# Kernel optimization log

Hardware: AMD Instinct MI355X
Metric: run time of the kernel (lower is better)

## Reference

```python
import jax, jax.numpy as jnp
import numpy as np

TAU = 1.0
SCALE = 0.5
LN_EPS = 1e-5
NORM_EPS = 1e-12


def setup_inputs() -> dict:
    key = jax.random.key(0)
    k1, = jax.random.split(key, 1)
    N, D = 16384, 128
    x = jax.random.normal(k1, (N, D), dtype=jnp.float32)
    gamma = jnp.ones((D,), dtype=jnp.float32)
    beta = jnp.zeros((D,), dtype=jnp.float32)
    return {"x": x, "gamma": gamma, "beta": beta}


def reference(x, gamma, beta):
    # 'cn' branch: row-normalize, full pairwise cosine sim, row softmax, aggregate
    norm = jnp.sqrt(jnp.sum(x * x, axis=1, keepdims=True))
    norm_x = x / jnp.maximum(norm, NORM_EPS)          # [N, D]
    sim = jax.nn.softmax(norm_x @ norm_x.T / TAU, axis=1)  # [N, N]
    x_neg = sim @ x                                    # [N, D]
    y = (1.0 + SCALE) * x - SCALE * x_neg
    # LayerNorm over the hidden dim
    mu = jnp.mean(y, axis=-1, keepdims=True)
    var = jnp.mean((y - mu) ** 2, axis=-1, keepdims=True)
    return (y - mu) * jax.lax.rsqrt(var + LN_EPS) * gamma + beta
```

## Files before the change

### kernel.cpp

```cpp
#include <hip/hip_runtime.h>
#include <stdint.h>

#define NN 16384
#define DD 128
#define KT 64
#define QB 256

typedef __bf16 bf16x8 __attribute__((ext_vector_type(8)));
typedef float f32x16 __attribute__((ext_vector_type(16)));
typedef uint32_t u32x4 __attribute__((ext_vector_type(4)));

using gv = __attribute__((address_space(1))) const void;
using lv = __attribute__((address_space(3))) void;

__device__ __forceinline__ uint16_t f2bf(float f) {
  uint32_t u = __builtin_bit_cast(uint32_t, f);
  u += 0x7fffu + ((u >> 16) & 1u);
  return (uint16_t)(u >> 16);
}

__global__ void k_norm(const float* __restrict__ x, uint16_t* __restrict__ nx) {
  const int wave = threadIdx.x >> 6, lane = threadIdx.x & 63;
  const int row = blockIdx.x * 4 + wave;
  const float2 v = *reinterpret_cast<const float2*>(x + (size_t)row * DD + 2 * lane);
  float ss = v.x * v.x + v.y * v.y;
#pragma unroll
  for (int m = 1; m < 64; m <<= 1) ss += __shfl_xor(ss, m);
  const float rn = 1.0f / fmaxf(sqrtf(ss), 1e-12f);
  uint32_t w = (uint32_t)f2bf(v.x * rn) | ((uint32_t)f2bf(v.y * rn) << 16);
  *reinterpret_cast<uint32_t*>(nx + (size_t)row * DD + 2 * lane) = w;
}

__global__ void k_transpose(const float* __restrict__ x, uint16_t* __restrict__ xT) {
  __shared__ uint16_t tile[64 * 65];
  const int r0 = (blockIdx.x >> 1) * 64;
  const int c0 = (blockIdx.x & 1) * 64;
  const int t = threadIdx.x;
#pragma unroll
  for (int e = 0; e < 16; ++e) {
    int idx = e * 256 + t;
    int r = idx >> 6, c = idx & 63;
    tile[r * 65 + c] = f2bf(x[(size_t)(r0 + r) * DD + c0 + c]);
  }
  __syncthreads();
#pragma unroll
  for (int e = 0; e < 16; ++e) {
    int idx = e * 256 + t;
    int cc = idx >> 6, rr = idx & 63;
    xT[(size_t)(c0 + cc) * NN + r0 + rr] = tile[rr * 65 + cc];
  }
}

__global__ __launch_bounds__(512, 2) void k_attn(
    const uint16_t* __restrict__ nx, const uint16_t* __restrict__ xT,
    float* __restrict__ Op, float* __restrict__ Lp, int nsplit) {
  __shared__ alignas(16) uint16_t Kb[3][KT * DD];
  __shared__ alignas(16) uint16_t Vb[3][DD * KT];

  const int tid = threadIdx.x;
  const int wave = tid >> 6;
  const int lane = tid & 63;
  const int rl = lane & 31;
  const int hi = lane >> 5;
  const int cswz = (16 * hi) ^ ((lane & 7) << 4);

  const int id = blockIdx.x;
  int qblock, split;
  if (nsplit == 4) { split = (id & 7) >> 1; qblock = ((id >> 3) << 1) | (id & 1); }
  else { qblock = id & 63; split = id >> 6; }

  const int nt = (NN / KT) / nsplit;
  const int t0s = split * nt;
  const int qw = qblock * QB + wave * 32;

  bf16x8 q8[8];
#pragma unroll
  for (int dc = 0; dc < 8; ++dc)
    q8[dc] = *reinterpret_cast<const bf16x8*>(
        nx + (size_t)(qw + rl) * DD + dc * 16 + 8 * hi);

  f32x16 o[4];
#pragma unroll
  for (int dt = 0; dt < 4; ++dt)
#pragma unroll
    for (int r = 0; r < 16; ++r) o[dt][r] = 0.f;
  float lsum = 0.f;

  const char* nxb = reinterpret_cast<const char*>(nx);
  const char* xtb = reinterpret_cast<const char*>(xT);

  auto stage = [&](int tt, int buf) {
    const int k0 = tt * KT;
#pragma unroll
    for (int jj = 0; jj < 2; ++jj) {
      const int j = wave * 2 + jj;
      const int A = j * 1024 + lane * 16;
      {
        const int row = A >> 8, b = A & 255;
        const char* src = nxb + (size_t)(k0 + row) * 256 + (b ^ ((row & 7) << 4));
        __builtin_amdgcn_global_load_lds((gv*)src,
            (lv*)(reinterpret_cast<char*>(&Kb[buf][0]) + j * 1024), 16, 0, 0);
      }
      {
        const int d = A >> 7, b2 = A & 127;
        const char* src = xtb + (size_t)d * (NN * 2) + (size_t)k0 * 2 + (b2 ^ ((d & 7) << 4));
        __builtin_amdgcn_global_load_lds((gv*)src,
            (lv*)(reinterpret_cast<char*>(&Vb[buf][0]) + j * 1024), 16, 0, 0);
      }
    }
  };

  stage(t0s + 0, 0);
  stage(t0s + 1, 1);

  for (int t = 0; t < nt; ++t) {
    __builtin_amdgcn_sched_barrier(0);
    if (t + 1 < nt) asm volatile("s_waitcnt vmcnt(4)" ::: "memory");
    else            asm volatile("s_waitcnt vmcnt(0)" ::: "memory");
    __builtin_amdgcn_s_barrier();
    __builtin_amdgcn_sched_barrier(0);
    if (t + 2 < nt) stage(t0s + t + 2, (t + 2) % 3);

    const int buf = t % 3;
    const char* kb = reinterpret_cast<const char*>(&Kb[buf][0]);
    const char* vb = reinterpret_cast<const char*>(&Vb[buf][0]);

    f32x16 s0, s1;
#pragma unroll
    for (int r = 0; r < 16; ++r) { s0[r] = 0.f; s1[r] = 0.f; }
#pragma unroll
    for (int dc = 0; dc < 8; ++dc) {
      const int byt = (dc * 32) ^ cswz;
      const bf16x8 ka0 = *reinterpret_cast<const bf16x8*>(kb + rl * 256 + byt);
      const bf16x8 ka1 = *reinterpret_cast<const bf16x8*>(kb + 8192 + rl * 256 + byt);
      s0 = __builtin_amdgcn_mfma_f32_32x32x16_bf16(ka0, q8[dc], s0, 0, 0, 0);
      s1 = __builtin_amdgcn_mfma_f32_32x32x16_bf16(ka1, q8[dc], s1, 0, 0, 0);
    }

    bf16x8 pa[4];
#pragma unroll
    for (int kt = 0; kt < 2; ++kt) {
      float pe[16];
#pragma unroll
      for (int r = 0; r < 16; ++r) {
        const float sv = (kt == 0) ? s0[r] : s1[r];
        pe[r] = __expf(sv);
        lsum += pe[r];
      }
#pragma unroll
      for (int kc = 0; kc < 2; ++kc) {
        uint32_t w0, w1, u0, u1;
        asm("v_cvt_pk_bf16_f32 %0, %1, %2" : "=v"(w0) : "v"(pe[8 * kc + 0]), "v"(pe[8 * kc + 1]));
        asm("v_cvt_pk_bf16_f32 %0, %1, %2" : "=v"(w1) : "v"(pe[8 * kc + 2]), "v"(pe[8 * kc + 3]));
        asm("v_cvt_pk_bf16_f32 %0, %1, %2" : "=v"(u0) : "v"(pe[8 * kc + 4]), "v"(pe[8 * kc + 5]));
        asm("v_cvt_pk_bf16_f32 %0, %1, %2" : "=v"(u1) : "v"(pe[8 * kc + 6]), "v"(pe[8 * kc + 7]));
        asm("v_permlane32_swap_b32 %0, %1" : "+v"(w0), "+v"(u0));
        asm("v_permlane32_swap_b32 %0, %1" : "+v"(w1), "+v"(u1));
        const u32x4 pd = {w0, w1, u0, u1};
        pa[kt * 2 + kc] = __builtin_bit_cast(bf16x8, pd);
      }
    }

#pragma unroll
    for (int c4 = 0; c4 < 4; ++c4) {
      const int byt = (c4 * 32) ^ cswz;
#pragma unroll
      for (int dt = 0; dt < 4; ++dt) {
        const bf16x8 vf = *reinterpret_cast<const bf16x8*>(vb + (dt * 32 + rl) * 128 + byt);
        o[dt] = __builtin_amdgcn_mfma_f32_32x32x16_bf16(pa[c4], vf, o[dt], 0, 0, 0);
      }
    }
  }

  const float lt = lsum + __shfl_xor(lsum, 32);
  if (hi == 0) Lp[(size_t)split * NN + qw + rl] = lt;

  float* Ob = Op + (size_t)split * NN * DD;
#pragma unroll
  for (int dt = 0; dt < 4; ++dt)
#pragma unroll
    for (int r = 0; r < 16; ++r) {
      const int q = (r & 3) + 8 * (r >> 2) + 4 * hi;
      Ob[(size_t)(qw + q) * DD + dt * 32 + rl] = o[dt][r];
    }
}

__global__ void k_final(const float* __restrict__ x, const float* __restrict__ gamma,
                        const float* __restrict__ beta, const float* __restrict__ Op,
                        const float* __restrict__ Lp, float* __restrict__ out, int nsplit) {
  const int wave = threadIdx.x >> 6, lane = threadIdx.x & 63;
  const int row = blockIdx.x * 4 + wave;
  float o0 = 0.f, o1 = 0.f, lt = 0.f;
  for (int s = 0; s < nsplit; ++s) {
    const float2 v = *reinterpret_cast<const float2*>(
        Op + (size_t)s * NN * DD + (size_t)row * DD + 2 * lane);
    o0 += v.x;
    o1 += v.y;
    lt += Lp[(size_t)s * NN + row];
  }
  const float inv = 1.0f / lt;
  const float2 xv = *reinterpret_cast<const float2*>(x + (size_t)row * DD + 2 * lane);
  float y0 = 1.5f * xv.x - 0.5f * o0 * inv;
  float y1 = 1.5f * xv.y - 0.5f * o1 * inv;
  float sum = y0 + y1;
#pragma unroll
  for (int m = 1; m < 64; m <<= 1) sum += __shfl_xor(sum, m);
  const float mu = sum * (1.0f / 128.0f);
  const float d0 = y0 - mu, d1 = y1 - mu;
  float vs = d0 * d0 + d1 * d1;
#pragma unroll
  for (int m = 1; m < 64; m <<= 1) vs += __shfl_xor(vs, m);
  const float rs = rsqrtf(vs * (1.0f / 128.0f) + 1e-5f);
  const float2 g = *reinterpret_cast<const float2*>(gamma + 2 * lane);
  const float2 b = *reinterpret_cast<const float2*>(beta + 2 * lane);
  float2 ov;
  ov.x = d0 * rs * g.x + b.x;
  ov.y = d1 * rs * g.y + b.y;
  *reinterpret_cast<float2*>(out + (size_t)row * DD + 2 * lane) = ov;
}

extern "C" void kernel_launch(void* const* d_in, const int* in_sizes, int n_in,
                              void* d_out, int out_size, void* d_ws, size_t ws_size,
                              hipStream_t stream) {
  const float* x = (const float*)d_in[0];
  const float* gamma = (const float*)d_in[1];
  const float* beta = (const float*)d_in[2];
  float* out = (float*)d_out;
  char* ws = (char*)d_ws;

  uint16_t* nx = (uint16_t*)ws;
  uint16_t* xT = (uint16_t*)(ws + (size_t)NN * DD * 2);
  const size_t base = (size_t)2 * NN * DD * 2;
  const size_t per = (size_t)NN * DD * 4 + (size_t)NN * 4;

  int nsplit = 1;
  if (ws_size >= base + 4 * per) nsplit = 4;
  else if (ws_size >= base + 2 * per) nsplit = 2;

  float* Op = (float*)(ws + base);
  float* Lp = (float*)(ws + base + (size_t)nsplit * NN * DD * 4);

  k_norm<<<NN / 4, 256, 0, stream>>>(x, nx);
  k_transpose<<<(NN / 64) * (DD / 64), 256, 0, stream>>>(x, xT);
  k_attn<<<dim3((NN / QB) * nsplit), 512, 0, stream>>>(nx, xT, Op, Lp, nsplit);
  k_final<<<NN / 4, 256, 0, stream>>>(x, gamma, beta, Op, Lp, out, nsplit);
}
```

Measured before the change: 159.1 us.

## Switch attention matmuls from bf16 to fp8 MFMA with halved block size

Normalized queries/keys, the transposed V and the softmax probabilities are now quantized to fp8 (e4m3) and both matmuls use the 32x32x16 fp8 MFMA, which halves LDS and global bytes per tile. The normalized vectors are scaled by a constant so that log2-domain exp can be taken directly with v_exp_f32. The query block shrinks to 128 rows with 256 threads and 3 blocks per CU, and the swizzles and split mapping are reworked to fit. s_setprio is raised around the MFMA sections. The cost is lower precision in the similarity scores and aggregated values, which risks accuracy failures.

```diff
diff --git a/kernel.cpp b/kernel.cpp
--- a/kernel.cpp
+++ b/kernel.cpp
@@ -4,80 +4,79 @@
 #define NN 16384
 #define DD 128
 #define KT 64
-#define QB 256
-
-typedef __bf16 bf16x8 __attribute__((ext_vector_type(8)));
+#define QB 128
+
 typedef float f32x16 __attribute__((ext_vector_type(16)));
-typedef uint32_t u32x4 __attribute__((ext_vector_type(4)));
+typedef long long i64;
 
 using gv = __attribute__((address_space(1))) const void;
 using lv = __attribute__((address_space(3))) void;
 
-__device__ __forceinline__ uint16_t f2bf(float f) {
-  uint32_t u = __builtin_bit_cast(uint32_t, f);
-  u += 0x7fffu + ((u >> 16) & 1u);
-  return (uint16_t)(u >> 16);
-}
-
-__global__ void k_norm(const float* __restrict__ x, uint16_t* __restrict__ nx) {
+__global__ void k_norm(const float* __restrict__ x, uint8_t* __restrict__ nx) {
   const int wave = threadIdx.x >> 6, lane = threadIdx.x & 63;
   const int row = blockIdx.x * 4 + wave;
   const float2 v = *reinterpret_cast<const float2*>(x + (size_t)row * DD + 2 * lane);
   float ss = v.x * v.x + v.y * v.y;
 #pragma unroll
   for (int m = 1; m < 64; m <<= 1) ss += __shfl_xor(ss, m);
-  const float rn = 1.0f / fmaxf(sqrtf(ss), 1e-12f);
-  uint32_t w = (uint32_t)f2bf(v.x * rn) | ((uint32_t)f2bf(v.y * rn) << 16);
-  *reinterpret_cast<uint32_t*>(nx + (size_t)row * DD + 2 * lane) = w;
-}
-
-__global__ void k_transpose(const float* __restrict__ x, uint16_t* __restrict__ xT) {
-  __shared__ uint16_t tile[64 * 65];
-  const int r0 = (blockIdx.x >> 1) * 64;
-  const int c0 = (blockIdx.x & 1) * 64;
+  const float rn = 1.2011224087f / fmaxf(sqrtf(ss), 1e-12f);
+  const int w = __builtin_amdgcn_cvt_pk_fp8_f32(v.x * rn, v.y * rn, 0, false);
+  *reinterpret_cast<uint16_t*>(nx + (size_t)row * DD + 2 * lane) = (uint16_t)w;
+}
+
+__global__ void k_transpose(const float* __restrict__ x, uint8_t* __restrict__ xT) {
+  __shared__ uint16_t tile[64 * 66];
+  const int n0 = blockIdx.x * 64;
   const int t = threadIdx.x;
 #pragma unroll
   for (int e = 0; e < 16; ++e) {
-    int idx = e * 256 + t;
-    int r = idx >> 6, c = idx & 63;
-    tile[r * 65 + c] = f2bf(x[(size_t)(r0 + r) * DD + c0 + c]);
+    const int idx = e * 256 + t;
+    const int r = idx >> 6, c2 = idx & 63;
+    const float2 v = *reinterpret_cast<const float2*>(x + (size_t)(n0 + r) * DD + 2 * c2);
+    const int w = __builtin_amdgcn_cvt_pk_fp8_f32(v.x, v.y, 0, false);
+    tile[r * 66 + c2] = (uint16_t)w;
   }
   __syncthreads();
-#pragma unroll
-  for (int e = 0; e < 16; ++e) {
-    int idx = e * 256 + t;
-    int cc = idx >> 6, rr = idx & 63;
-    xT[(size_t)(c0 + cc) * NN + r0 + rr] = tile[rr * 65 + cc];
-  }
-}
-
-__global__ __launch_bounds__(512, 2) void k_attn(
-    const uint16_t* __restrict__ nx, const uint16_t* __restrict__ xT,
+  const uint8_t* t8 = reinterpret_cast<const uint8_t*>(tile);
+#pragma unroll
+  for (int e = 0; e < 8; ++e) {
+    const int idx = e * 256 + t;
+    const int d = idx >> 4, n4 = (idx & 15) << 2;
+    uint32_t w = (uint32_t)t8[(n4 + 0) * 132 + d];
+    w |= (uint32_t)t8[(n4 + 1) * 132 + d] << 8;
+    w |= (uint32_t)t8[(n4 + 2) * 132 + d] << 16;
+    w |= (uint32_t)t8[(n4 + 3) * 132 + d] << 24;
+    *reinterpret_cast<uint32_t*>(xT + (size_t)d * NN + n0 + n4) = w;
+  }
+}
+
+__global__ __launch_bounds__(256, 3) void k_attn(
+    const uint8_t* __restrict__ nx, const uint8_t* __restrict__ xT,
     float* __restrict__ Op, float* __restrict__ Lp, int nsplit) {
-  __shared__ alignas(16) uint16_t Kb[3][KT * DD];
-  __shared__ alignas(16) uint16_t Vb[3][DD * KT];
+  __shared__ alignas(16) uint8_t Kb[3][KT * DD];
+  __shared__ alignas(16) uint8_t Vb[3][DD * KT];
 
   const int tid = threadIdx.x;
   const int wave = tid >> 6;
   const int lane = tid & 63;
   const int rl = lane & 31;
   const int hi = lane >> 5;
-  const int cswz = (16 * hi) ^ ((lane & 7) << 4);
+  const int swzk = (rl & 7) << 4;
+  const int swzv = ((rl >> 1) & 3) << 4;
 
   const int id = blockIdx.x;
-  int qblock, split;
-  if (nsplit == 4) { split = (id & 7) >> 1; qblock = ((id >> 3) << 1) | (id & 1); }
-  else { qblock = id & 63; split = id >> 6; }
+  const int gs = 8 / nsplit;
+  const int split = (id & 7) / gs;
+  const int qblock = (id >> 3) * gs + (id & (gs - 1));
 
   const int nt = (NN / KT) / nsplit;
   const int t0s = split * nt;
   const int qw = qblock * QB + wave * 32;
 
-  bf16x8 q8[8];
+  i64 q8[8];
 #pragma unroll
   for (int dc = 0; dc < 8; ++dc)
-    q8[dc] = *reinterpret_cast<const bf16x8*>(
-        nx + (size_t)(qw + rl) * DD + dc * 16 + 8 * hi);
+    q8[dc] = *reinterpret_cast<const i64*>(nx + (size_t)(qw + rl) * DD + dc * 16 + 8 * hi);
 
   f32x16 o[4];
 #pragma unroll
@@ -85,9 +84,6 @@
 #pragma unroll
     for (int r = 0; r < 16; ++r) o[dt][r] = 0.f;
   float lsum = 0.f;
-
-  const char* nxb = reinterpret_cast<const char*>(nx);
-  const char* xtb = reinterpret_cast<const char*>(xT);
 
   auto stage = [&](int tt, int buf) {
     const int k0 = tt * KT;
@@ -96,16 +92,16 @@
       const int j = wave * 2 + jj;
       const int A = j * 1024 + lane * 16;
       {
-        const int row = A >> 8, b = A & 255;
-        const char* src = nxb + (size_t)(k0 + row) * 256 + (b ^ ((row & 7) << 4));
+        const int row = A >> 7, b = A & 127;
+        const uint8_t* src = nx + (size_t)(k0 + row) * DD + (b ^ ((row & 7) << 4));
         __builtin_amdgcn_global_load_lds((gv*)src,
-            (lv*)(reinterpret_cast<char*>(&Kb[buf][0]) + j * 1024), 16, 0, 0);
+            (lv*)(&Kb[buf][0] + j * 1024), 16, 0, 0);
       }
       {
-        const int d = A >> 7, b2 = A & 127;
-        const char* src = xtb + (size_t)d * (NN * 2) + (size_t)k0 * 2 + (b2 ^ ((d & 7) << 4));
+        const int d = A >> 6, b2 = A & 63;
+        const uint8_t* src = xT + (size_t)d * NN + k0 + (b2 ^ (((d >> 1) & 3) << 4));
         __builtin_amdgcn_global_load_lds((gv*)src,
-            (lv*)(reinterpret_cast<char*>(&Vb[buf][0]) + j * 1024), 16, 0, 0);
+            (lv*)(&Vb[buf][0] + j * 1024), 16, 0, 0);
       }
     }
   };
@@ -122,54 +118,59 @@
     if (t + 2 < nt) stage(t0s + t + 2, (t + 2) % 3);
 
     const int buf = t % 3;
-    const char* kb = reinterpret_cast<const char*>(&Kb[buf][0]);
-    const char* vb = reinterpret_cast<const char*>(&Vb[buf][0]);
+    const uint8_t* kb = &Kb[buf][0];
+    const uint8_t* vb = &Vb[buf][0];
 
     f32x16 s0, s1;
 #pragma unroll
     for (int r = 0; r < 16; ++r) { s0[r] = 0.f; s1[r] = 0.f; }
+    __builtin_amdgcn_s_setprio(1);
 #pragma unroll
     for (int dc = 0; dc < 8; ++dc) {
-      const int byt = (dc * 32) ^ cswz;
-      const bf16x8 ka0 = *reinterpret_cast<const bf16x8*>(kb + rl * 256 + byt);
-      const bf16x8 ka1 = *reinterpret_cast<const bf16x8*>(kb + 8192 + rl * 256 + byt);
-      s0 = __builtin_amdgcn_mfma_f32_32x32x16_bf16(ka0, q8[dc], s0, 0, 0, 0);
-      s1 = __builtin_amdgcn_mfma_f32_32x32x16_bf16(ka1, q8[dc], s1, 0, 0, 0);
-    }
-
-    bf16x8 pa[4];
+      const int byt = (dc * 16 + 8 * hi) ^ swzk;
+      const i64 ka0 = __builtin_bit_cast(i64, *reinterpret_cast<const uint2*>(kb + rl * 128 + byt));
+      const i64 ka1 = __builtin_bit_cast(i64, *reinterpret_cast<const uint2*>(kb + 4096 + rl * 128 + byt));
+      s0 = __builtin_amdgcn_mfma_f32_32x32x16_fp8_fp8(ka0, q8[dc], s0, 0, 0, 0);
+      s1 = __builtin_amdgcn_mfma_f32_32x32x16_fp8_fp8(ka1, q8[dc], s1, 0, 0, 0);
+    }
+    __builtin_amdgcn_s_setprio(0);
+
+    i64 pa[4];
 #pragma unroll
     for (int kt = 0; kt < 2; ++kt) {
       float pe[16];
 #pragma unroll
       for (int r = 0; r < 16; ++r) {
         const float sv = (kt == 0) ? s0[r] : s1[r];
-        pe[r] = __expf(sv);
-        lsum += pe[r];
+        float p;
+        asm("v_exp_f32 %0, %1" : "=v"(p) : "v"(sv));
+        pe[r] = p;
+        lsum += p;
       }
 #pragma unroll
       for (int kc = 0; kc < 2; ++kc) {
-        uint32_t w0, w1, u0, u1;
-        asm("v_cvt_pk_bf16_f32 %0, %1, %2" : "=v"(w0) : "v"(pe[8 * kc + 0]), "v"(pe[8 * kc + 1]));
-        asm("v_cvt_pk_bf16_f32 %0, %1, %2" : "=v"(w1) : "v"(pe[8 * kc + 2]), "v"(pe[8 * kc + 3]));
-        asm("v_cvt_pk_bf16_f32 %0, %1, %2" : "=v"(u0) : "v"(pe[8 * kc + 4]), "v"(pe[8 * kc + 5]));
-        asm("v_cvt_pk_bf16_f32 %0, %1, %2" : "=v"(u1) : "v"(pe[8 * kc + 6]), "v"(pe[8 * kc + 7]));
-        asm("v_permlane32_swap_b32 %0, %1" : "+v"(w0), "+v"(u0));
-        asm("v_permlane32_swap_b32 %0, %1" : "+v"(w1), "+v"(u1));
-        const u32x4 pd = {w0, w1, u0, u1};
-        pa[kt * 2 + kc] = __builtin_bit_cast(bf16x8, pd);
-      }
-    }
-
+        uint32_t wlo = (uint32_t)__builtin_amdgcn_cvt_pk_fp8_f32(pe[8 * kc + 0], pe[8 * kc + 1], 0, false);
+        wlo = (uint32_t)__builtin_amdgcn_cvt_pk_fp8_f32(pe[8 * kc + 2], pe[8 * kc + 3], (int)wlo, true);
+        uint32_t whi = (uint32_t)__builtin_amdgcn_cvt_pk_fp8_f32(pe[8 * kc + 4], pe[8 * kc + 5], 0, false);
+        whi = (uint32_t)__builtin_amdgcn_cvt_pk_fp8_f32(pe[8 * kc + 6], pe[8 * kc + 7], (int)whi, true);
+        asm("v_permlane32_swap_b32 %0, %1" : "+v"(wlo), "+v"(whi));
+        const uint2 pd = {wlo, whi};
+        pa[kt * 2 + kc] = __builtin_bit_cast(i64, pd);
+      }
+    }
+
+    __builtin_amdgcn_s_setprio(1);
 #pragma unroll
     for (int c4 = 0; c4 < 4; ++c4) {
-      const int byt = (c4 * 32) ^ cswz;
+      const int cb = (c4 * 16 + 8 * hi) ^ swzv;
 #pragma unroll
       for (int dt = 0; dt < 4; ++dt) {
-        const bf16x8 vf = *reinterpret_cast<const bf16x8*>(vb + (dt * 32 + rl) * 128 + byt);
-        o[dt] = __builtin_amdgcn_mfma_f32_32x32x16_bf16(pa[c4], vf, o[dt], 0, 0, 0);
-      }
-    }
+        const i64 vf = __builtin_bit_cast(i64,
+            *reinterpret_cast<const uint2*>(vb + (dt * 32 + rl) * 64 + cb));
+        o[dt] = __builtin_amdgcn_mfma_f32_32x32x16_fp8_fp8(pa[c4], vf, o[dt], 0, 0, 0);
+      }
+    }
+    __builtin_amdgcn_s_setprio(0);
   }
 
   const float lt = lsum + __shfl_xor(lsum, 32);
@@ -228,9 +229,9 @@
   float* out = (float*)d_out;
   char* ws = (char*)d_ws;
 
-  uint16_t* nx = (uint16_t*)ws;
-  uint16_t* xT = (uint16_t*)(ws + (size_t)NN * DD * 2);
-  const size_t base = (size_t)2 * NN * DD * 2;
+  uint8_t* nx = (uint8_t*)ws;
+  uint8_t* xT = (uint8_t*)(ws + (size_t)NN * DD);
+  const size_t base = (size_t)2 * NN * DD;
   const size_t per = (size_t)NN * DD * 4 + (size_t)NN * 4;
 
   int nsplit = 1;
@@ -241,7 +242,7 @@
   float* Lp = (float*)(ws + base + (size_t)nsplit * NN * DD * 4);
 
   k_norm<<<NN / 4, 256, 0, stream>>>(x, nx);
-  k_transpose<<<(NN / 64) * (DD / 64), 256, 0, stream>>>(x, xT);
-  k_attn<<<dim3((NN / QB) * nsplit), 512, 0, stream>>>(nx, xT, Op, Lp, nsplit);
+  k_transpose<<<NN / 64, 256, 0, stream>>>(x, xT);
+  k_attn<<<dim3((NN / QB) * nsplit), 256, 0, stream>>>(nx, xT, Op, Lp, nsplit);
   k_final<<<NN / 4, 256, 0, stream>>>(x, gamma, beta, Op, Lp, out, nsplit);
 }
```

Result: faster. 133.1 us (-16.4%).
